# Optimization experiments

Measured on AMD Instinct MI355X. Metric: run time of the kernel, lower is better.

The kernel has to match this reference:

```python
import jax, jax.numpy as jnp
import numpy as np

DIM = 192
HEADS = 6
WH, WW = 8, 8
N = WH * WW
B_ = 2048
NW = 512


def _relative_position_index():
    coords = np.stack(np.meshgrid(np.arange(WH), np.arange(WW), indexing='ij'))  # 2,Wh,Ww
    cf = coords.reshape(2, -1)
    rel = cf[:, :, None] - cf[:, None, :]  # 2,N,N
    rel = rel.transpose(1, 2, 0).astype(np.int32)
    rel[:, :, 0] += WH - 1
    rel[:, :, 1] += WW - 1
    rel[:, :, 0] *= 2 * WW - 1
    return jnp.asarray(rel.sum(-1))  # N,N int32


def setup_inputs() -> dict:
    key = jax.random.key(0)
    ks = jax.random.split(key, 16)
    s = 0.02
    inp = {
        'q': jax.random.normal(ks[0], (B_, N, DIM), jnp.float32),
        'k': jax.random.normal(ks[1], (B_, N, DIM), jnp.float32),
        'v': jax.random.normal(ks[2], (B_, N, DIM), jnp.float32),
        'mask': jax.random.normal(ks[3], (NW, N, N), jnp.float32),
        'attn_mask': jax.random.randint(ks[4], (B_, 1, N, N), 0, 2).astype(bool),
        'Wq': jax.random.normal(ks[5], (DIM, DIM), jnp.float32) * s,
        'bq': jnp.zeros((DIM,), jnp.float32),
        'Wk': jax.random.normal(ks[6], (DIM, DIM), jnp.float32) * s,
        'bk': jnp.zeros((DIM,), jnp.float32),
        'Wv': jax.random.normal(ks[7], (DIM, DIM), jnp.float32) * s,
        'bv': jnp.zeros((DIM,), jnp.float32),
        'Wp': jax.random.normal(ks[8], (DIM, DIM), jnp.float32) * s,
        'bp': jnp.zeros((DIM,), jnp.float32),
        'rpb_table': jax.random.normal(ks[9], ((2 * WH - 1) * (2 * WW - 1), HEADS), jnp.float32) * s,
        'rel_idx': _relative_position_index(),
    }
    return inp


def reference(q, k, v, mask, attn_mask, Wq, bq, Wk, bk, Wv, bv, Wp, bp, rpb_table, rel_idx):
    Bw, n, C = q.shape
    hd = C // HEADS
    scale = hd ** (-0.5)
    # linear projections (torch Linear: x @ W.T + b), split heads -> b h n d
    qh = (q @ Wq.T + bq).reshape(Bw, n, HEADS, hd).transpose(0, 2, 1, 3) * scale
    kh = (k @ Wk.T + bk).reshape(Bw, n, HEADS, hd).transpose(0, 2, 1, 3)
    vh = (v @ Wv.T + bv).reshape(Bw, n, HEADS, hd).transpose(0, 2, 1, 3)
    attn = jnp.einsum('bhnd,bhmd->bhnm', qh, kh)  # (B_, H, N, N)
    attn = jnp.where(attn_mask, jnp.float32(-1e9), attn)
    # relative position bias gather: (N,N,H) -> (H,N,N)
    bias = rpb_table[rel_idx.reshape(-1)].reshape(n, n, HEADS).transpose(2, 0, 1)
    attn = attn + bias[None]
    nW = mask.shape[0]
    attn = attn.reshape(Bw // nW, nW, HEADS, n, n) + mask[None, :, None]
    attn = jax.nn.softmax(attn.reshape(Bw, HEADS, n, n), axis=-1)
    x = jnp.einsum('bhnm,bhmd->bhnd', attn, vh).transpose(0, 2, 1, 3).reshape(Bw, n, C)
    return x @ Wp.T + bp
```

## Files before the change

### kernel.cpp

```cpp
#include <hip/hip_runtime.h>

#define DIM    192
#define HEADS  6
#define HD     32
#define NTOK   64
#define NWIN   512
#define NBLK   2048
#define TPB    384
#define XPITCH 200
#define MPITCH 65
#define WMAT   (DIM*DIM)

typedef short  bf16x4 __attribute__((ext_vector_type(4)));
typedef short  bf16x8 __attribute__((ext_vector_type(8)));
typedef float  f32x4  __attribute__((ext_vector_type(4)));

#if defined(__HIP_DEVICE_COMPILE__)
#if !__has_builtin(__builtin_amdgcn_mfma_f32_16x16x32_bf16)
#error "missing __builtin_amdgcn_mfma_f32_16x16x32_bf16"
#endif
#if !__has_builtin(__builtin_amdgcn_mfma_f32_16x16x16bf16_1k)
#error "missing __builtin_amdgcn_mfma_f32_16x16x16bf16_1k"
#endif
#endif

static __device__ __forceinline__ unsigned short f2bf(float f){
  unsigned u = __builtin_bit_cast(unsigned, f);
  u += 0x7FFFu + ((u >> 16) & 1u);
  return (unsigned short)(u >> 16);
}

static __device__ __forceinline__ f32x4 mfma32(bf16x8 a, bf16x8 b, f32x4 c){
  return __builtin_amdgcn_mfma_f32_16x16x32_bf16(a, b, c, 0, 0, 0);
}
static __device__ __forceinline__ f32x4 mfma16(bf16x4 a, bf16x4 b, f32x4 c){
  return __builtin_amdgcn_mfma_f32_16x16x16bf16_1k(a, b, c, 0, 0, 0);
}

static __device__ __forceinline__ bf16x8 wfrag(const unsigned short* __restrict__ W, int row, int k0){
  return *(const bf16x8*)(W + row*DIM + k0);
}

static __device__ __forceinline__ uint2 pack_bf(const float4 f){
  uint2 u;
  u.x = (unsigned)f2bf(f.x) | ((unsigned)f2bf(f.y) << 16);
  u.y = (unsigned)f2bf(f.z) | ((unsigned)f2bf(f.w) << 16);
  return u;
}

static __device__ __forceinline__ void stage_xin(unsigned short* xt, const float* __restrict__ src, int t){
  #pragma unroll
  for (int j = 0; j < 8; ++j){
    const int i4  = t + j*TPB;
    const float4 f = ((const float4*)src)[i4];
    const int row = i4 / 48;
    const int col = (i4 - row*48) * 4;
    *(uint2*)(xt + row*XPITCH + col) = pack_bf(f);
  }
}

__global__ void detect_amask_kernel(const unsigned int* __restrict__ am, int* __restrict__ mode){
  __shared__ int sawFloat, sawByte;
  if (threadIdx.x == 0){ sawFloat = 0; sawByte = 0; }
  __syncthreads();
  const uint4 ld = ((const uint4*)am)[threadIdx.x];
  unsigned w[4] = {ld.x, ld.y, ld.z, ld.w};
  int f = 0, bm = 0;
  #pragma unroll
  for (int i = 0; i < 4; ++i){
    if (w[i] == 0x3F800000u) f = 1;
    else if (w[i] & ~1u)     bm = 1;
  }
  if (f)  atomicOr(&sawFloat, 1);
  if (bm) atomicOr(&sawByte, 1);
  __syncthreads();
  if (threadIdx.x == 0) *mode = sawFloat ? 2 : (sawByte ? 1 : 0);
}

__global__ void bias_pre_kernel(const float* __restrict__ rpb, const int* __restrict__ rel_idx,
                                float* __restrict__ bias_pre){
  const int e = blockIdx.x*256 + threadIdx.x;
  if (e >= HEADS*NTOK*NTOK) return;
  const int rest = e & 4095, m = rest >> 6, n = rest & 63;
  bias_pre[e] = rpb[rel_idx[n*NTOK + m]*HEADS + (e >> 12)];
}

__global__ void wconv_kernel(const float* __restrict__ Wq, const float* __restrict__ Wk,
                             const float* __restrict__ Wv, const float* __restrict__ Wp,
                             unsigned short* __restrict__ wbf){
  const int e4 = blockIdx.x*256 + threadIdx.x;
  if (e4 >= 4*WMAT/4) return;
  const int mat = e4 / (WMAT/4);
  const int off = e4 - mat*(WMAT/4);
  const float* src = (mat==0)?Wq:(mat==1)?Wk:(mat==2)?Wv:Wp;
  const float4 f = ((const float4*)src)[off];
  unsigned short* dst = wbf + mat*WMAT + off*4;
  dst[0]=f2bf(f.x); dst[1]=f2bf(f.y); dst[2]=f2bf(f.z); dst[3]=f2bf(f.w);
}

__global__ __launch_bounds__(TPB, 3) void swin_kernel(
  const float* __restrict__ q, const float* __restrict__ kin, const float* __restrict__ vin,
  const float* __restrict__ mask, const void* __restrict__ amask,
  const unsigned short* __restrict__ wbf,
  const float* __restrict__ bq, const float* __restrict__ bk,
  const float* __restrict__ bv, const float* __restrict__ bp,
  const float* __restrict__ bias_pre, const int* __restrict__ mflag,
  float* __restrict__ out)
{
  __shared__ unsigned short xa[NTOK * XPITCH];
  __shared__ unsigned short xb[NTOK * XPITCH];
  __shared__ float madd[NTOK * MPITCH];

  const int b    = blockIdx.x;
  const int t    = threadIdx.x;
  const int h    = t >> 6;
  const int lane = t & 63;
  const int l15  = lane & 15;
  const int g    = lane >> 4;
  const int c0   = h * HD;
  const size_t base = (size_t)b * (NTOK * DIM);
  const float scale = 0.17677669529663687f;
  const f32x4 fz = {0.f, 0.f, 0.f, 0.f};

  const unsigned short* Wq = wbf;
  const unsigned short* Wk = wbf + WMAT;
  const unsigned short* Wv = wbf + 2*WMAT;
  const unsigned short* Wp = wbf + 3*WMAT;

  {
    const int mode = mflag[0];
    const float* mrow = mask + (size_t)(b & (NWIN-1)) * (NTOK*NTOK);
    const size_t abase = (size_t)b * (NTOK*NTOK);
    for (int i = t; i < NTOK*NTOK; i += TPB){
      const int n = i >> 6, m = i & 63;
      bool msk;
      if (mode == 0)      msk = ((const int*)amask)[abase + i] != 0;
      else if (mode == 1) msk = ((const unsigned char*)amask)[abase + i] != 0;
      else                msk = ((const float*)amask)[abase + i] != 0.0f;
      madd[m*MPITCH + n] = mrow[i] + (msk ? -1e9f : 0.0f);
    }
    stage_xin(xa, q + base, t);
    stage_xin(xb, kin + base, t);
  }
  __syncthreads();

  bf16x4 Qf[4][2], Kf[4][2], Vf[2][4];

  float4 vpre[8];
  #pragma unroll
  for (int j = 0; j < 8; ++j) vpre[j] = ((const float4*)(vin + base))[t + j*TPB];

  {
    f32x4 acc[2][4];
    #pragma unroll
    for (int a0=0;a0<2;++a0){
      #pragma unroll
      for (int a1=0;a1<4;++a1) acc[a0][a1] = fz;
    }
    #pragma unroll
    for (int kt = 0; kt < 6; ++kt){
      const int k0 = kt*32 + g*8;
      const bf16x8 w0 = wfrag(Wq, c0 + l15, k0);
      const bf16x8 w1 = wfrag(Wq, c0 + 16 + l15, k0);
      #pragma unroll
      for (int nt = 0; nt < 4; ++nt){
        const bf16x8 xf = *(const bf16x8*)(xa + (nt*16 + l15)*XPITCH + k0);
        acc[0][nt] = mfma32(w0, xf, acc[0][nt]);
        acc[1][nt] = mfma32(w1, xf, acc[1][nt]);
      }
    }
    #pragma unroll
    for (int dt = 0; dt < 2; ++dt){
      const float4 bb = *(const float4*)(bq + c0 + dt*16 + g*4);
      #pragma unroll
      for (int nt = 0; nt < 4; ++nt){
        bf16x4 f;
        f[0]=(short)f2bf((acc[dt][nt][0]+bb.x)*scale);
        f[1]=(short)f2bf((acc[dt][nt][1]+bb.y)*scale);
        f[2]=(short)f2bf((acc[dt][nt][2]+bb.z)*scale);
        f[3]=(short)f2bf((acc[dt][nt][3]+bb.w)*scale);
        Qf[nt][dt] = f;
      }
    }
  }
  {
    f32x4 acc[2][4];
    #pragma unroll
    for (int a0=0;a0<2;++a0){
      #pragma unroll
      for (int a1=0;a1<4;++a1) acc[a0][a1] = fz;
    }
    #pragma unroll
    for (int kt = 0; kt < 6; ++kt){
      const int k0 = kt*32 + g*8;
      const bf16x8 w0 = wfrag(Wk, c0 + l15, k0);
      const bf16x8 w1 = wfrag(Wk, c0 + 16 + l15, k0);
      #pragma unroll
      for (int mt = 0; mt < 4; ++mt){
        const bf16x8 xf = *(const bf16x8*)(xb + (mt*16 + l15)*XPITCH + k0);
        acc[0][mt] = mfma32(w0, xf, acc[0][mt]);
        acc[1][mt] = mfma32(w1, xf, acc[1][mt]);
      }
    }
    #pragma unroll
    for (int dt = 0; dt < 2; ++dt){
      const float4 bb = *(const float4*)(bk + c0 + dt*16 + g*4);
      #pragma unroll
      for (int mt = 0; mt < 4; ++mt){
        bf16x4 f;
        f[0]=(short)f2bf(acc[dt][mt][0]+bb.x);
        f[1]=(short)f2bf(acc[dt][mt][1]+bb.y);
        f[2]=(short)f2bf(acc[dt][mt][2]+bb.z);
        f[3]=(short)f2bf(acc[dt][mt][3]+bb.w);
        Kf[mt][dt] = f;
      }
    }
  }
  __syncthreads();

  #pragma unroll
  for (int j = 0; j < 8; ++j){
    const int i4  = t + j*TPB;
    const int row = i4 / 48;
    const int col = (i4 - row*48) * 4;
    *(uint2*)(xa + row*XPITCH + col) = pack_bf(vpre[j]);
  }
  __syncthreads();

  {
    f32x4 acc[4][2];
    #pragma unroll
    for (int a0=0;a0<4;++a0){
      #pragma unroll
      for (int a1=0;a1<2;++a1) acc[a0][a1] = fz;
    }
    #pragma unroll
    for (int kt = 0; kt < 6; ++kt){
      const int k0 = kt*32 + g*8;
      const bf16x8 w0 = wfrag(Wv, c0 + l15, k0);
      const bf16x8 w1 = wfrag(Wv, c0 + 16 + l15, k0);
      #pragma unroll
      for (int mt = 0; mt < 4; ++mt){
        const bf16x8 xf = *(const bf16x8*)(xa + (mt*16 + l15)*XPITCH + k0);
        acc[mt][0] = mfma32(xf, w0, acc[mt][0]);
        acc[mt][1] = mfma32(xf, w1, acc[mt][1]);
      }
    }
    const float bv0 = bv[c0 + l15];
    const float bv1 = bv[c0 + 16 + l15];
    #pragma unroll
    for (int mt = 0; mt < 4; ++mt){
      bf16x4 f0, f1;
      f0[0]=(short)f2bf(acc[mt][0][0]+bv0); f0[1]=(short)f2bf(acc[mt][0][1]+bv0);
      f0[2]=(short)f2bf(acc[mt][0][2]+bv0); f0[3]=(short)f2bf(acc[mt][0][3]+bv0);
      f1[0]=(short)f2bf(acc[mt][1][0]+bv1); f1[1]=(short)f2bf(acc[mt][1][1]+bv1);
      f1[2]=(short)f2bf(acc[mt][1][2]+bv1); f1[3]=(short)f2bf(acc[mt][1][3]+bv1);
      Vf[0][mt] = f0;
      Vf[1][mt] = f1;
    }
  }

  f32x4 s[4][4];
  #pragma unroll
  for (int mt = 0; mt < 4; ++mt){
    #pragma unroll
    for (int nt = 0; nt < 4; ++nt){
      f32x4 a = mfma16(Kf[mt][0], Qf[nt][0], fz);
      s[mt][nt] = mfma16(Kf[mt][1], Qf[nt][1], a);
    }
  }

  const float* bh = bias_pre + h * (NTOK*NTOK);
  bf16x4 Pf[4][4];
  #pragma unroll
  for (int nt = 0; nt < 4; ++nt){
    const int n = nt*16 + l15;
    float mx = -3.0e38f;
    #pragma unroll
    for (int mt = 0; mt < 4; ++mt){
      #pragma unroll
      for (int r = 0; r < 4; ++r){
        const int m = mt*16 + g*4 + r;
        const float val = s[mt][nt][r] + madd[m*MPITCH + n] + bh[m*64 + n];
        s[mt][nt][r] = val;
        mx = fmaxf(mx, val);
      }
    }
    mx = fmaxf(mx, __shfl_xor(mx, 16, 64));
    mx = fmaxf(mx, __shfl_xor(mx, 32, 64));
    float sum = 0.f;
    #pragma unroll
    for (int mt = 0; mt < 4; ++mt){
      #pragma unroll
      for (int r = 0; r < 4; ++r){
        const float e = __expf(s[mt][nt][r] - mx);
        s[mt][nt][r] = e;
        sum += e;
      }
    }
    sum += __shfl_xor(sum, 16, 64);
    sum += __shfl_xor(sum, 32, 64);
    const float inv = 1.0f / sum;
    #pragma unroll
    for (int ms = 0; ms < 4; ++ms){
      bf16x4 f;
      f[0]=(short)f2bf(s[ms][nt][0]*inv); f[1]=(short)f2bf(s[ms][nt][1]*inv);
      f[2]=(short)f2bf(s[ms][nt][2]*inv); f[3]=(short)f2bf(s[ms][nt][3]*inv);
      Pf[nt][ms] = f;
    }
  }

  f32x4 o[2][4];
  #pragma unroll
  for (int a0=0;a0<2;++a0){
    #pragma unroll
    for (int a1=0;a1<4;++a1) o[a0][a1] = fz;
  }
  #pragma unroll
  for (int ms = 0; ms < 4; ++ms){
    #pragma unroll
    for (int dt = 0; dt < 2; ++dt){
      #pragma unroll
      for (int nt = 0; nt < 4; ++nt){
        o[dt][nt] = mfma16(Vf[dt][ms], Pf[nt][ms], o[dt][nt]);
      }
    }
  }

  #pragma unroll
  for (int dt = 0; dt < 2; ++dt){
    #pragma unroll
    for (int nt = 0; nt < 4; ++nt){
      const int n   = nt*16 + l15;
      const int col = c0 + dt*16 + g*4;
      uint2 u;
      u.x = (unsigned)f2bf(o[dt][nt][0]) | ((unsigned)f2bf(o[dt][nt][1]) << 16);
      u.y = (unsigned)f2bf(o[dt][nt][2]) | ((unsigned)f2bf(o[dt][nt][3]) << 16);
      *(uint2*)(xb + n*XPITCH + col) = u;
    }
  }
  __syncthreads();

  {
    f32x4 acc[4][2];
    #pragma unroll
    for (int a0=0;a0<4;++a0){
      #pragma unroll
      for (int a1=0;a1<2;++a1) acc[a0][a1] = fz;
    }
    #pragma unroll
    for (int kt = 0; kt < 6; ++kt){
      const int k0 = kt*32 + g*8;
      const bf16x8 w0 = wfrag(Wp, c0 + l15, k0);
      const bf16x8 w1 = wfrag(Wp, c0 + 16 + l15, k0);
      #pragma unroll
      for (int nt = 0; nt < 4; ++nt){
        const bf16x8 xf = *(const bf16x8*)(xb + (nt*16 + l15)*XPITCH + k0);
        acc[nt][0] = mfma32(xf, w0, acc[nt][0]);
        acc[nt][1] = mfma32(xf, w1, acc[nt][1]);
      }
    }
    const float bp0 = bp[c0 + l15];
    const float bp1 = bp[c0 + 16 + l15];
    #pragma unroll
    for (int nt = 0; nt < 4; ++nt){
      #pragma unroll
      for (int ctl = 0; ctl < 2; ++ctl){
        const int c = c0 + ctl*16 + l15;
        const float badd = ctl ? bp1 : bp0;
        #pragma unroll
        for (int r = 0; r < 4; ++r){
          const int n = nt*16 + g*4 + r;
          out[base + (size_t)(n*DIM + c)] = acc[nt][ctl][r] + badd;
        }
      }
    }
  }
}

extern "C" void kernel_launch(void* const* d_in, const int* in_sizes, int n_in,
                              void* d_out, int out_size, void* d_ws, size_t ws_size,
                              hipStream_t stream){
  const float* q     = (const float*)d_in[0];
  const float* k     = (const float*)d_in[1];
  const float* v     = (const float*)d_in[2];
  const float* mask  = (const float*)d_in[3];
  const void*  amask = d_in[4];
  const float* Wq    = (const float*)d_in[5];
  const float* bq    = (const float*)d_in[6];
  const float* Wk    = (const float*)d_in[7];
  const float* bk    = (const float*)d_in[8];
  const float* Wv    = (const float*)d_in[9];
  const float* bv    = (const float*)d_in[10];
  const float* Wp    = (const float*)d_in[11];
  const float* bp    = (const float*)d_in[12];
  const float* rpb   = (const float*)d_in[13];
  const int*   ridx  = (const int*)d_in[14];
  float* out = (float*)d_out;

  float*          bias_pre = (float*)d_ws;
  int*            mflag    = (int*)((char*)d_ws + 98304);
  unsigned short* wbf      = (unsigned short*)((char*)d_ws + 98560);

  detect_amask_kernel<<<1, 256, 0, stream>>>((const unsigned int*)amask, mflag);
  bias_pre_kernel<<<96, 256, 0, stream>>>(rpb, ridx, bias_pre);
  wconv_kernel<<<144, 256, 0, stream>>>(Wq, Wk, Wv, Wp, wbf);
  swin_kernel<<<NBLK, TPB, 0, stream>>>(q, k, v, mask, amask, wbf,
                                        bq, bk, bv, bp,
                                        bias_pre, mflag, out);
}
```

Measured before the change: 378.0 us.

## Load Q/K/V projection fragments directly from global memory instead of LDS staging

Removes the shared-memory staging of the fp32 q/k/v inputs. Each wave now reads its bf16 MFMA fragments straight from global memory and converts them on the fly. This eliminates one LDS buffer, several barriers and the register-held V prefetch, cutting LDS footprint and synchronization. In exchange, every head wave re-reads the whole input tile from cache and repeats the fp32-to-bf16 conversion, multiplying global/L2 traffic and conversion ALU work.

```diff
diff --git a/kernel.cpp b/kernel.cpp
--- a/kernel.cpp
+++ b/kernel.cpp
@@ -41,22 +41,13 @@
   return *(const bf16x8*)(W + row*DIM + k0);
 }
 
-static __device__ __forceinline__ uint2 pack_bf(const float4 f){
-  uint2 u;
-  u.x = (unsigned)f2bf(f.x) | ((unsigned)f2bf(f.y) << 16);
-  u.y = (unsigned)f2bf(f.z) | ((unsigned)f2bf(f.w) << 16);
-  return u;
-}
-
-static __device__ __forceinline__ void stage_xin(unsigned short* xt, const float* __restrict__ src, int t){
-  #pragma unroll
-  for (int j = 0; j < 8; ++j){
-    const int i4  = t + j*TPB;
-    const float4 f = ((const float4*)src)[i4];
-    const int row = i4 / 48;
-    const int col = (i4 - row*48) * 4;
-    *(uint2*)(xt + row*XPITCH + col) = pack_bf(f);
-  }
+static __device__ __forceinline__ bf16x8 xfrag(const float* __restrict__ X, int row, int k0){
+  const float4 a = *(const float4*)(X + row*DIM + k0);
+  const float4 b = *(const float4*)(X + row*DIM + k0 + 4);
+  bf16x8 r;
+  r[0]=(short)f2bf(a.x); r[1]=(short)f2bf(a.y); r[2]=(short)f2bf(a.z); r[3]=(short)f2bf(a.w);
+  r[4]=(short)f2bf(b.x); r[5]=(short)f2bf(b.y); r[6]=(short)f2bf(b.z); r[7]=(short)f2bf(b.w);
+  return r;
 }
 
 __global__ void detect_amask_kernel(const unsigned int* __restrict__ am, int* __restrict__ mode){
@@ -107,8 +98,7 @@
   const float* __restrict__ bias_pre, const int* __restrict__ mflag,
   float* __restrict__ out)
 {
-  __shared__ unsigned short xa[NTOK * XPITCH];
-  __shared__ unsigned short xb[NTOK * XPITCH];
+  __shared__ unsigned short xout[NTOK * XPITCH];
   __shared__ float madd[NTOK * MPITCH];
 
   const int b    = blockIdx.x;
@@ -126,6 +116,9 @@
   const unsigned short* Wk = wbf + WMAT;
   const unsigned short* Wv = wbf + 2*WMAT;
   const unsigned short* Wp = wbf + 3*WMAT;
+  const float* qb = q   + base;
+  const float* kb = kin + base;
+  const float* vb = vin + base;
 
   {
     const int mode = mflag[0];
@@ -139,16 +132,9 @@
       else                msk = ((const float*)amask)[abase + i] != 0.0f;
       madd[m*MPITCH + n] = mrow[i] + (msk ? -1e9f : 0.0f);
     }
-    stage_xin(xa, q + base, t);
-    stage_xin(xb, kin + base, t);
-  }
-  __syncthreads();
+  }
 
   bf16x4 Qf[4][2], Kf[4][2], Vf[2][4];
-
-  float4 vpre[8];
-  #pragma unroll
-  for (int j = 0; j < 8; ++j) vpre[j] = ((const float4*)(vin + base))[t + j*TPB];
 
   {
     f32x4 acc[2][4];
@@ -164,7 +150,7 @@
       const bf16x8 w1 = wfrag(Wq, c0 + 16 + l15, k0);
       #pragma unroll
       for (int nt = 0; nt < 4; ++nt){
-        const bf16x8 xf = *(const bf16x8*)(xa + (nt*16 + l15)*XPITCH + k0);
+        const bf16x8 xf = xfrag(qb, nt*16 + l15, k0);
         acc[0][nt] = mfma32(w0, xf, acc[0][nt]);
         acc[1][nt] = mfma32(w1, xf, acc[1][nt]);
       }
@@ -197,7 +183,7 @@
       const bf16x8 w1 = wfrag(Wk, c0 + 16 + l15, k0);
       #pragma unroll
       for (int mt = 0; mt < 4; ++mt){
-        const bf16x8 xf = *(const bf16x8*)(xb + (mt*16 + l15)*XPITCH + k0);
+        const bf16x8 xf = xfrag(kb, mt*16 + l15, k0);
         acc[0][mt] = mfma32(w0, xf, acc[0][mt]);
         acc[1][mt] = mfma32(w1, xf, acc[1][mt]);
       }
@@ -216,17 +202,6 @@
       }
     }
   }
-  __syncthreads();
-
-  #pragma unroll
-  for (int j = 0; j < 8; ++j){
-    const int i4  = t + j*TPB;
-    const int row = i4 / 48;
-    const int col = (i4 - row*48) * 4;
-    *(uint2*)(xa + row*XPITCH + col) = pack_bf(vpre[j]);
-  }
-  __syncthreads();
-
   {
     f32x4 acc[4][2];
     #pragma unroll
@@ -241,7 +216,7 @@
       const bf16x8 w1 = wfrag(Wv, c0 + 16 + l15, k0);
       #pragma unroll
       for (int mt = 0; mt < 4; ++mt){
-        const bf16x8 xf = *(const bf16x8*)(xa + (mt*16 + l15)*XPITCH + k0);
+        const bf16x8 xf = xfrag(vb, mt*16 + l15, k0);
         acc[mt][0] = mfma32(xf, w0, acc[mt][0]);
         acc[mt][1] = mfma32(xf, w1, acc[mt][1]);
       }
@@ -270,6 +245,8 @@
     }
   }
 
+  __syncthreads();
+
   const float* bh = bias_pre + h * (NTOK*NTOK);
   bf16x4 Pf[4][4];
   #pragma unroll
@@ -336,7 +313,7 @@
       uint2 u;
       u.x = (unsigned)f2bf(o[dt][nt][0]) | ((unsigned)f2bf(o[dt][nt][1]) << 16);
       u.y = (unsigned)f2bf(o[dt][nt][2]) | ((unsigned)f2bf(o[dt][nt][3]) << 16);
-      *(uint2*)(xb + n*XPITCH + col) = u;
+      *(uint2*)(xout + n*XPITCH + col) = u;
     }
   }
   __syncthreads();
@@ -355,7 +332,7 @@
       const bf16x8 w1 = wfrag(Wp, c0 + 16 + l15, k0);
       #pragma unroll
       for (int nt = 0; nt < 4; ++nt){
-        const bf16x8 xf = *(const bf16x8*)(xb + (nt*16 + l15)*XPITCH + k0);
+        const bf16x8 xf = *(const bf16x8*)(xout + (nt*16 + l15)*XPITCH + k0);
         acc[nt][0] = mfma32(xf, w0, acc[nt][0]);
         acc[nt][1] = mfma32(xf, w1, acc[nt][1]);
       }
```

After: 520.7 us. +37.8%, slower.
